# Optimization experiments

Measured on AMD Instinct MI355X. Metric: run time of the kernel, lower is better.

Reference implementation:

```python
import jax, jax.numpy as jnp
import numpy as np

EPS = 1e-3  # matches MaskedBatchNorm2d default eps=0.001


def setup_inputs() -> dict:
    key = jax.random.key(0)
    k1, k2 = jax.random.split(key)
    B, C, W, H = 16, 64, 256, 256
    x = jax.random.normal(k1, (B, C, W, H), dtype=jnp.float32)
    # densified sparse-voxel feature maps the module is designed for.
    keep = (jax.random.uniform(k2, (B, W, H)) < 0.3).astype(jnp.float32)
    x = x * keep[:, None, :, :]
    return {"x": x}


def reference(x):
    """Faithful masked batchnorm (training mode, affine=False).

    Original: per-batch nonzero() of channel-sum, pad index lists to the max
    count with zeros (i.e. duplicate location (0,0)), gather [B, Nmax, C],
    compute per-channel mean/var over ALL gathered entries (padding included),
    divide by sqrt(var+eps) (mean NOT subtracted in output), scatter back to
    nonzero locations — padded rows also overwrite location (0,0).
    """
    B, C, W, H = x.shape
    x1 = x.sum(axis=1)                      # [B, W, H]
    m = x1 != 0                             # nonzero-site mask
    mf = m.astype(x.dtype)
    n = mf.sum(axis=(1, 2))                 # nonzero count per batch item [B]
    Nmax = n.max()
    pad = Nmax - n                          # number of padded (0,0) duplicates per item
    total = (B * Nmax).astype(x.dtype)      # B * max(num_nonzeros)

    x00 = x[:, :, 0, 0]                     # [B, C] value gathered by padded indices

    # per-channel mean over masked sites + padded duplicates of (0,0)
    sum_c = jnp.einsum('bcwh,bwh->c', x, mf) + jnp.einsum('bc,b->c', x00, pad)
    mean = sum_c / total                    # [C]

    d = x - mean[None, :, None, None]
    var = (jnp.einsum('bcwh,bwh->c', d * d, mf)
           + jnp.einsum('bc,b->c', (x00 - mean[None, :]) ** 2, pad)) / total

    inv = 1.0 / jnp.sqrt(var + EPS)         # [C]; note: mean is NOT subtracted
    xn = x * inv[None, :, None, None]

    out = jnp.where(m[:, None, :, :], xn, x)
    # padded scatter rows write normalized x[b,:,0,0] into location (0,0)
    has_pad = (pad > 0)[:, None]            # [B,1]
    out = out.at[:, :, 0, 0].set(jnp.where(has_pad, x00 * inv[None, :], out[:, :, 0, 0]))
    return out
```

## Files before the change

### kernel.cpp

```cpp
#include <hip/hip_runtime.h>


#define NB 16
#define CB 64
#define WH 65536
#define TILE 256
#define NTILES (NB * WH / TILE)
#define GRID1 1024
#define TPT (NTILES / GRID1)
#define DIRTY_CAP 512
#define EPS 0.001f


__global__ __launch_bounds__(256, 4)
void mbn_pass1(const float* __restrict__ x, float* __restrict__ sqPart,
               unsigned* __restrict__ nPart, unsigned* __restrict__ dirtyCnt,
               int* __restrict__ dirtyLoc) {
    __shared__ float lds_s[4][TILE];
    __shared__ float lds_a[4][TILE];
    __shared__ unsigned cnt_lds[16];
    const int tid  = threadIdx.x;
    const int wave = tid >> 6;
    const int lane = tid & 63;
    if (tid < 16) cnt_lds[tid] = 0;

    float sAcc[16], qAcc[16];
#pragma unroll
    for (int j = 0; j < 16; ++j) { sAcc[j] = 0.f; qAcc[j] = 0.f; }
    __syncthreads();

    for (int tt = 0; tt < TPT; ++tt) {
        const int tile = blockIdx.x + tt * GRID1;
        const int b    = tile >> 8;
        const int whb  = (tile & 255) * TILE;
        const float* base = x + (((size_t)(b * 64 + wave * 16)) << 16) + whb + lane * 4;

        float sp0 = 0.f, sp1 = 0.f, sp2 = 0.f, sp3 = 0.f;
        float aa0 = 0.f, aa1 = 0.f, aa2 = 0.f, aa3 = 0.f;
#pragma unroll
        for (int j = 0; j < 16; ++j) {
            float4 v = *(const float4*)(base + ((size_t)j << 16));
            sp0 += v.x; sp1 += v.y; sp2 += v.z; sp3 += v.w;
            aa0 += fabsf(v.x); aa1 += fabsf(v.y); aa2 += fabsf(v.z); aa3 += fabsf(v.w);
            sAcc[j] += (v.x + v.y) + (v.z + v.w);
            qAcc[j] = fmaf(v.x, v.x, qAcc[j]);
            qAcc[j] = fmaf(v.y, v.y, qAcc[j]);
            qAcc[j] = fmaf(v.z, v.z, qAcc[j]);
            qAcc[j] = fmaf(v.w, v.w, qAcc[j]);
        }
        *(float4*)&lds_s[wave][lane * 4] = make_float4(sp0, sp1, sp2, sp3);
        *(float4*)&lds_a[wave][lane * 4] = make_float4(aa0, aa1, aa2, aa3);
        __syncthreads();

        float s = lds_s[0][tid] + lds_s[1][tid] + lds_s[2][tid] + lds_s[3][tid];
        float a = lds_a[0][tid] + lds_a[1][tid] + lds_a[2][tid] + lds_a[3][tid];
        bool mask = (s != 0.0f);
        unsigned long long bal = __ballot(mask);
        if (lane == 0) atomicAdd(&cnt_lds[b], (unsigned)__popcll(bal));
        if (!mask && a != 0.0f) {
            unsigned idx = atomicAdd(dirtyCnt, 1u);
            if (idx < DIRTY_CAP) dirtyLoc[idx] = (b << 16) | (whb + tid);
        }
        __syncthreads();
    }

#pragma unroll
    for (int j = 0; j < 16; ++j) {
        float sv = sAcc[j], qv = qAcc[j];
        for (int off = 32; off; off >>= 1) {
            sv += __shfl_xor(sv, off);
            qv += __shfl_xor(qv, off);
        }
        if (lane == 0) {
            sqPart[blockIdx.x * 128 + wave * 16 + j]      = sv;
            sqPart[blockIdx.x * 128 + 64 + wave * 16 + j] = qv;
        }
    }
    __syncthreads();
    if (tid < 16) nPart[blockIdx.x * 16 + tid] = cnt_lds[tid];
}

__global__ void mbn_finalize(const float* __restrict__ x, const float* __restrict__ sqPart,
                             const unsigned* __restrict__ nPart,
                             const unsigned* __restrict__ dirtyCnt, const int* __restrict__ dirtyLoc,
                             float* __restrict__ inv, int* __restrict__ padOut) {
    __shared__ float red[256];
    __shared__ float sq[128];
    __shared__ unsigned npar[4][16];
    __shared__ unsigned ntot[16];
    const int t = threadIdx.x;
    const int idx = t & 127, half = t >> 7;

    float acc = 0.f;
    const float* p = sqPart + (size_t)half * 512 * 128 + idx;
#pragma unroll 8
    for (int blk = 0; blk < 512; ++blk) acc += p[(size_t)blk * 128];
    red[t] = acc;

    if (t >= 192) {
        const int b = t & 15, q = (t >> 4) & 3;
        unsigned s = 0;
        const unsigned* np = nPart + q * 256 * 16 + b;
#pragma unroll 8
        for (int blk = 0; blk < 256; ++blk) s += np[blk * 16];
        npar[q][b] = s;
    }
    __syncthreads();
    if (t < 128) sq[t] = red[t] + red[t + 128];
    if (t < 16)  ntot[t] = npar[0][t] + npar[1][t] + npar[2][t] + npar[3][t];
    __syncthreads();

    if (t < 64) {
        const int c = t;
        unsigned nmax = 0;
#pragma unroll
        for (int b = 0; b < NB; ++b) { unsigned nb = ntot[b]; nmax = nb > nmax ? nb : nmax; }
        const float total = (float)(16u * nmax);

        float s = sq[c], q = sq[64 + c];
        unsigned cnt = *dirtyCnt; if (cnt > DIRTY_CAP) cnt = DIRTY_CAP;
        for (unsigned i = 0; i < cnt; ++i) {
            int loc = dirtyLoc[i];
            int b = loc >> 16, wh = loc & 65535;
            float v = x[(((size_t)(b * 64 + c)) << 16) + wh];
            s -= v; q -= v * v;
        }
        float p1 = 0.f, p2 = 0.f;
#pragma unroll
        for (int b = 0; b < NB; ++b) {
            float padf = (float)(nmax - ntot[b]);
            float v00  = x[((size_t)(b * 64 + c)) << 16];
            p1 = fmaf(padf, v00, p1);
            p2 = fmaf(padf, v00 * v00, p2);
            if (c == 0) padOut[b] = (int)(nmax - ntot[b]);
        }
        float mean = (s + p1) / total;
        float var  = (q + p2) / total - mean * mean;
        inv[c] = 1.0f / sqrtf(var + EPS);
    }
}

__global__ __launch_bounds__(256)
void mbn_pass2(const float4* __restrict__ x4, float4* __restrict__ out4,
               const float* __restrict__ inv) {
    const int blk = blockIdx.x;
    const float sc = inv[(blk >> 3) & 63];
    const size_t base = (size_t)blk * 2048 + threadIdx.x;
#pragma unroll
    for (int k = 0; k < 8; ++k) {
        size_t i = base + (size_t)k * 256;
        float4 v = x4[i];
        v.x *= sc; v.y *= sc; v.z *= sc; v.w *= sc;
        out4[i] = v;
    }
}

__global__ void mbn_fixup(const float* __restrict__ x, float* __restrict__ out,
                          const unsigned* __restrict__ dirtyCnt, const int* __restrict__ dirtyLoc,
                          const int* __restrict__ padArr) {
    const int c = threadIdx.x;
    unsigned cnt = *dirtyCnt; if (cnt > DIRTY_CAP) cnt = DIRTY_CAP;
    for (unsigned i = 0; i < cnt; ++i) {
        int loc = dirtyLoc[i];
        int b = loc >> 16, wh = loc & 65535;
        if (wh == 0 && padArr[b] > 0) continue;
        size_t idx = (((size_t)(b * 64 + c)) << 16) + wh;
        out[idx] = x[idx];
    }
}

extern "C" void kernel_launch(void* const* d_in, const int* in_sizes, int n_in,
                              void* d_out, int out_size, void* d_ws, size_t ws_size,
                              hipStream_t stream) {
    const float* x = (const float*)d_in[0];
    float* out = (float*)d_out;
    float* wsf = (float*)d_ws;

    float*    sqPart   = wsf;
    unsigned* nPart    = (unsigned*)(wsf + 131072);
    unsigned* dirtyCnt = (unsigned*)(wsf + 147456);
    float*    inv      = wsf + 147520;
    int*      padArr   = (int*)(wsf + 147584);
    int*      dirtyLoc = (int*)(wsf + 147600);

    hipMemsetAsync((char*)d_ws + 147456 * 4, 0, 64, stream);

    mbn_pass1<<<GRID1, 256, 0, stream>>>(x, sqPart, nPart, dirtyCnt, dirtyLoc);
    mbn_finalize<<<1, 256, 0, stream>>>(x, sqPart, nPart, dirtyCnt, dirtyLoc, inv, padArr);
    mbn_pass2<<<8192, 256, 0, stream>>>((const float4*)x, (float4*)out, inv);
    mbn_fixup<<<1, 64, 0, stream>>>(x, out, dirtyCnt, dirtyLoc, padArr);
}
```

Before: 593.9 us.

## Fuse fixup into pass2, batch pass1 tiles, widen finalize, use nontemporal stores

Pass1 now processes two tiles per barrier pair with double-buffered LDS and requests higher occupancy. Finalize is parallelized over 1024 threads to shorten the serial reduction. The separate fixup kernel is folded into pass2, where each block patches the dirty locations in its own segment. Pass2 writes its output with nontemporal vector stores. Together these aim to cut launch overhead, barrier count and the single-block tail, at the cost of more register pressure and an extra dirtyCnt read in every pass2 block.

Result: slower. 724.9 us (+22.1%).

```diff
diff --git a/kernel.cpp b/kernel.cpp
--- a/kernel.cpp
+++ b/kernel.cpp
@@ -11,13 +11,15 @@
 #define DIRTY_CAP 512
 #define EPS 0.001f
 
-
-__global__ __launch_bounds__(256, 4)
+typedef float f32x4 __attribute__((ext_vector_type(4)));
+
+
+__global__ __launch_bounds__(256, 8)
 void mbn_pass1(const float* __restrict__ x, float* __restrict__ sqPart,
                unsigned* __restrict__ nPart, unsigned* __restrict__ dirtyCnt,
                int* __restrict__ dirtyLoc) {
-    __shared__ float lds_s[4][TILE];
-    __shared__ float lds_a[4][TILE];
+    __shared__ float lds_s[2][4][TILE];
+    __shared__ float lds_a[2][4][TILE];
     __shared__ unsigned cnt_lds[16];
     const int tid  = threadIdx.x;
     const int wave = tid >> 6;
@@ -29,37 +31,45 @@
     for (int j = 0; j < 16; ++j) { sAcc[j] = 0.f; qAcc[j] = 0.f; }
     __syncthreads();
 
-    for (int tt = 0; tt < TPT; ++tt) {
-        const int tile = blockIdx.x + tt * GRID1;
-        const int b    = tile >> 8;
-        const int whb  = (tile & 255) * TILE;
-        const float* base = x + (((size_t)(b * 64 + wave * 16)) << 16) + whb + lane * 4;
-
-        float sp0 = 0.f, sp1 = 0.f, sp2 = 0.f, sp3 = 0.f;
-        float aa0 = 0.f, aa1 = 0.f, aa2 = 0.f, aa3 = 0.f;
-#pragma unroll
-        for (int j = 0; j < 16; ++j) {
-            float4 v = *(const float4*)(base + ((size_t)j << 16));
-            sp0 += v.x; sp1 += v.y; sp2 += v.z; sp3 += v.w;
-            aa0 += fabsf(v.x); aa1 += fabsf(v.y); aa2 += fabsf(v.z); aa3 += fabsf(v.w);
-            sAcc[j] += (v.x + v.y) + (v.z + v.w);
-            qAcc[j] = fmaf(v.x, v.x, qAcc[j]);
-            qAcc[j] = fmaf(v.y, v.y, qAcc[j]);
-            qAcc[j] = fmaf(v.z, v.z, qAcc[j]);
-            qAcc[j] = fmaf(v.w, v.w, qAcc[j]);
-        }
-        *(float4*)&lds_s[wave][lane * 4] = make_float4(sp0, sp1, sp2, sp3);
-        *(float4*)&lds_a[wave][lane * 4] = make_float4(aa0, aa1, aa2, aa3);
+    for (int g = 0; g < 2; ++g) {
+#pragma unroll
+        for (int sub = 0; sub < 2; ++sub) {
+            const int tile = blockIdx.x + (g * 2 + sub) * GRID1;
+            const int b    = tile >> 8;
+            const int whb  = (tile & 255) * TILE;
+            const float* base = x + (((size_t)(b * 64 + wave * 16)) << 16) + whb + lane * 4;
+
+            float sp0 = 0.f, sp1 = 0.f, sp2 = 0.f, sp3 = 0.f;
+            float aa0 = 0.f, aa1 = 0.f, aa2 = 0.f, aa3 = 0.f;
+#pragma unroll
+            for (int j = 0; j < 16; ++j) {
+                float4 v = *(const float4*)(base + ((size_t)j << 16));
+                sp0 += v.x; sp1 += v.y; sp2 += v.z; sp3 += v.w;
+                aa0 += fabsf(v.x); aa1 += fabsf(v.y); aa2 += fabsf(v.z); aa3 += fabsf(v.w);
+                sAcc[j] += (v.x + v.y) + (v.z + v.w);
+                qAcc[j] = fmaf(v.x, v.x, qAcc[j]);
+                qAcc[j] = fmaf(v.y, v.y, qAcc[j]);
+                qAcc[j] = fmaf(v.z, v.z, qAcc[j]);
+                qAcc[j] = fmaf(v.w, v.w, qAcc[j]);
+            }
+            *(float4*)&lds_s[sub][wave][lane * 4] = make_float4(sp0, sp1, sp2, sp3);
+            *(float4*)&lds_a[sub][wave][lane * 4] = make_float4(aa0, aa1, aa2, aa3);
+        }
         __syncthreads();
 
-        float s = lds_s[0][tid] + lds_s[1][tid] + lds_s[2][tid] + lds_s[3][tid];
-        float a = lds_a[0][tid] + lds_a[1][tid] + lds_a[2][tid] + lds_a[3][tid];
-        bool mask = (s != 0.0f);
-        unsigned long long bal = __ballot(mask);
-        if (lane == 0) atomicAdd(&cnt_lds[b], (unsigned)__popcll(bal));
-        if (!mask && a != 0.0f) {
-            unsigned idx = atomicAdd(dirtyCnt, 1u);
-            if (idx < DIRTY_CAP) dirtyLoc[idx] = (b << 16) | (whb + tid);
+#pragma unroll
+        for (int sub = 0; sub < 2; ++sub) {
+            const int tile = blockIdx.x + (g * 2 + sub) * GRID1;
+            const int b    = tile >> 8;
+            float s = lds_s[sub][0][tid] + lds_s[sub][1][tid] + lds_s[sub][2][tid] + lds_s[sub][3][tid];
+            float a = lds_a[sub][0][tid] + lds_a[sub][1][tid] + lds_a[sub][2][tid] + lds_a[sub][3][tid];
+            bool mask = (s != 0.0f);
+            unsigned long long bal = __ballot(mask);
+            if (lane == 0) atomicAdd(&cnt_lds[b], (unsigned)__popcll(bal));
+            if (!mask && a != 0.0f) {
+                unsigned idx = atomicAdd(dirtyCnt, 1u);
+                if (idx < DIRTY_CAP) dirtyLoc[idx] = (b << 16) | ((tile & 255) * TILE + tid);
+            }
         }
         __syncthreads();
     }
@@ -76,38 +86,48 @@
             sqPart[blockIdx.x * 128 + 64 + wave * 16 + j] = qv;
         }
     }
-    __syncthreads();
     if (tid < 16) nPart[blockIdx.x * 16 + tid] = cnt_lds[tid];
 }
 
-__global__ void mbn_finalize(const float* __restrict__ x, const float* __restrict__ sqPart,
-                             const unsigned* __restrict__ nPart,
-                             const unsigned* __restrict__ dirtyCnt, const int* __restrict__ dirtyLoc,
-                             float* __restrict__ inv, int* __restrict__ padOut) {
-    __shared__ float red[256];
+__global__ __launch_bounds__(1024)
+void mbn_finalize(const float* __restrict__ x, const float* __restrict__ sqPart,
+                  const unsigned* __restrict__ nPart,
+                  const unsigned* __restrict__ dirtyCnt, const int* __restrict__ dirtyLoc,
+                  float* __restrict__ inv, int* __restrict__ padOut) {
+    __shared__ float red[1024];
     __shared__ float sq[128];
-    __shared__ unsigned npar[4][16];
+    __shared__ unsigned npar[16][16];
     __shared__ unsigned ntot[16];
     const int t = threadIdx.x;
-    const int idx = t & 127, half = t >> 7;
+    const int col = t & 127, grp = t >> 7;
 
     float acc = 0.f;
-    const float* p = sqPart + (size_t)half * 512 * 128 + idx;
+    const float* p = sqPart + (size_t)grp * 128 * 128 + col;
 #pragma unroll 8
-    for (int blk = 0; blk < 512; ++blk) acc += p[(size_t)blk * 128];
+    for (int r = 0; r < 128; ++r) acc += p[(size_t)r * 128];
     red[t] = acc;
 
-    if (t >= 192) {
-        const int b = t & 15, q = (t >> 4) & 3;
+    if (t < 256) {
+        const int b = t & 15, g2 = t >> 4;
         unsigned s = 0;
-        const unsigned* np = nPart + q * 256 * 16 + b;
+        const unsigned* np = nPart + g2 * 64 * 16 + b;
 #pragma unroll 8
-        for (int blk = 0; blk < 256; ++blk) s += np[blk * 16];
-        npar[q][b] = s;
+        for (int r = 0; r < 64; ++r) s += np[r * 16];
+        npar[g2][b] = s;
     }
     __syncthreads();
-    if (t < 128) sq[t] = red[t] + red[t + 128];
-    if (t < 16)  ntot[t] = npar[0][t] + npar[1][t] + npar[2][t] + npar[3][t];
+    if (t < 128) {
+        float v = 0.f;
+#pragma unroll
+        for (int g2 = 0; g2 < 8; ++g2) v += red[g2 * 128 + t];
+        sq[t] = v;
+    }
+    if (t < 16) {
+        unsigned v = 0;
+#pragma unroll
+        for (int g2 = 0; g2 < 16; ++g2) v += npar[g2][t];
+        ntot[t] = v;
+    }
     __syncthreads();
 
     if (t < 64) {
@@ -141,31 +161,38 @@
 }
 
 __global__ __launch_bounds__(256)
-void mbn_pass2(const float4* __restrict__ x4, float4* __restrict__ out4,
-               const float* __restrict__ inv) {
+void mbn_pass2(const float* __restrict__ x, float* __restrict__ out,
+               const float* __restrict__ inv, const unsigned* __restrict__ dirtyCnt,
+               const int* __restrict__ dirtyLoc, const int* __restrict__ padArr) {
     const int blk = blockIdx.x;
     const float sc = inv[(blk >> 3) & 63];
+    const f32x4* x4 = (const f32x4*)x;
+    f32x4* out4 = (f32x4*)out;
     const size_t base = (size_t)blk * 2048 + threadIdx.x;
 #pragma unroll
     for (int k = 0; k < 8; ++k) {
         size_t i = base + (size_t)k * 256;
-        float4 v = x4[i];
-        v.x *= sc; v.y *= sc; v.z *= sc; v.w *= sc;
-        out4[i] = v;
-    }
-}
-
-__global__ void mbn_fixup(const float* __restrict__ x, float* __restrict__ out,
-                          const unsigned* __restrict__ dirtyCnt, const int* __restrict__ dirtyLoc,
-                          const int* __restrict__ padArr) {
-    const int c = threadIdx.x;
-    unsigned cnt = *dirtyCnt; if (cnt > DIRTY_CAP) cnt = DIRTY_CAP;
-    for (unsigned i = 0; i < cnt; ++i) {
-        int loc = dirtyLoc[i];
-        int b = loc >> 16, wh = loc & 65535;
-        if (wh == 0 && padArr[b] > 0) continue;
-        size_t idx = (((size_t)(b * 64 + c)) << 16) + wh;
-        out[idx] = x[idx];
+        f32x4 v = x4[i];
+        v *= sc;
+        __builtin_nontemporal_store(v, &out4[i]);
+    }
+
+    unsigned cnt = *dirtyCnt;
+    if (cnt != 0) {
+        __syncthreads();
+        if (threadIdx.x == 0) {
+            if (cnt > DIRTY_CAP) cnt = DIRTY_CAP;
+            const int bb = blk >> 9, cc = (blk >> 3) & 63, seg = blk & 7;
+            const int lo = seg * 8192, hi = lo + 8192;
+            for (unsigned i = 0; i < cnt; ++i) {
+                int loc = dirtyLoc[i];
+                int b = loc >> 16, wh = loc & 65535;
+                if (b != bb || wh < lo || wh >= hi) continue;
+                if (wh == 0 && padArr[b] > 0) continue;
+                size_t idx = (((size_t)(b * 64 + cc)) << 16) + wh;
+                out[idx] = x[idx];
+            }
+        }
     }
 }
 
@@ -186,7 +213,6 @@
     hipMemsetAsync((char*)d_ws + 147456 * 4, 0, 64, stream);
 
     mbn_pass1<<<GRID1, 256, 0, stream>>>(x, sqPart, nPart, dirtyCnt, dirtyLoc);
-    mbn_finalize<<<1, 256, 0, stream>>>(x, sqPart, nPart, dirtyCnt, dirtyLoc, inv, padArr);
-    mbn_pass2<<<8192, 256, 0, stream>>>((const float4*)x, (float4*)out, inv);
-    mbn_fixup<<<1, 64, 0, stream>>>(x, out, dirtyCnt, dirtyLoc, padArr);
-}
+    mbn_finalize<<<1, 1024, 0, stream>>>(x, sqPart, nPart, dirtyCnt, dirtyLoc, inv, padArr);
+    mbn_pass2<<<8192, 256, 0, stream>>>(x, out, inv, dirtyCnt, dirtyLoc, padArr);
+}
```
